# Optimization experiments

Hardware: AMD Instinct MI355X
Metric: run time of the kernel (lower is better)

## Reference

```python
import jax, jax.numpy as jnp
import numpy as np

VOCAB, D, E, I, L, B, T = 32000, 1024, 8, 2048, 2, 4, 2048
LN_EPS = 1e-5


def setup_inputs() -> dict:
    key = jax.random.key(0)
    ks = jax.random.split(key, 10)
    return {
        "x": jax.random.randint(ks[0], (B, T), 0, VOCAB),
        "emb": jax.random.normal(ks[1], (VOCAB, D), jnp.float32) * 0.02,
        "ln_g": jnp.ones((L, D), jnp.float32),
        "ln_b": jnp.zeros((L, D), jnp.float32),
        "gate_w": jax.random.normal(ks[2], (L, D, E), jnp.float32) * 0.02,
        "gate_b": jnp.zeros((L, E), jnp.float32),
        "w1": jax.random.normal(ks[3], (L, E, D, I), jnp.float32) * 0.02,
        "w2": jax.random.normal(ks[4], (L, E, I, D), jnp.float32) * 0.02,
        "head_w": jax.random.normal(ks[5], (D, VOCAB), jnp.float32) * 0.02,
        "head_b": jnp.zeros((VOCAB,), jnp.float32),
    }


def _layer_norm(h, g, b):
    mu = jnp.mean(h, axis=-1, keepdims=True)
    var = jnp.mean(jnp.square(h - mu), axis=-1, keepdims=True)
    return (h - mu) * jax.lax.rsqrt(var + LN_EPS) * g + b


def reference(x, emb, ln_g, ln_b, gate_w, gate_b, w1, w2, head_w, head_b):
    h = emb[x]  # [B,T,D]
    experts_all = []
    for l in range(ln_g.shape[0]):  # small fixed layer loop
        xn = _layer_norm(h, ln_g[l], ln_b[l])
        gating_logits = xn @ gate_w[l] + gate_b[l]          # [B,T,E]
        rw = jax.nn.softmax(gating_logits, axis=-1)
        e = jnp.einsum('btc,eci->btei', xn, w1[l])           # [B,T,E,I]
        e = jax.nn.gelu(e, approximate=False)                # torch F.gelu default = erf
        eo = jnp.einsum('btei,eic->btec', e, w2[l])          # [B,T,E,D]
        agg = jnp.einsum('btec,bte->btc', eo, rw)
        h = h + agg
        experts_all.append(eo)
    logits = h @ head_w + head_b                             # [B,T,VOCAB]
    return logits, jnp.stack(experts_all)                    # [L,B,T,E,D]
```

## Files before the change

kernel.cpp:

```cpp
#include <hip/hip_runtime.h>
#include <hip/hip_bf16.h>
#include <stdint.h>

#define NTOK 8192
#define DM   1024
#define NE   8
#define DI   2048
#define NL   2
#define NV   32000

typedef __attribute__((ext_vector_type(8))) __bf16 bf16x8;
typedef __attribute__((ext_vector_type(4))) float  f32x4;
typedef unsigned short u16;

__device__ __forceinline__ u16 f2bf(float f) {
  uint32_t u = __builtin_bit_cast(uint32_t, f);
  return (u16)((u + 0x7fffu + ((u >> 16) & 1u)) >> 16);
}

__device__ __forceinline__ void gload_lds16(const u16* g, void* l) {
  __builtin_amdgcn_global_load_lds(
      (const __attribute__((address_space(1))) void*)g,
      (__attribute__((address_space(3))) void*)l, 16, 0, 0);
}

__device__ __forceinline__ int xcd_swz(int orig, int nwg) {
  const int x = orig & 7, i = orig >> 3;
  const int q = nwg >> 3, r = nwg & 7;
  return (x < r ? x * (q + 1) : r * (q + 1) + (x - r) * q) + i;
}

template <int EPI>
__global__ __launch_bounds__(256, 2) void k_gemm(
    const u16* __restrict__ A0, const u16* __restrict__ W0,
    void* __restrict__ O0, const float* __restrict__ bias,
    int K, int mBlks, int nBlks,
    size_t aStride, size_t wStride, size_t oStride, int ldOut) {
  extern __shared__ char lds[];
  const int logical = xcd_swz(blockIdx.x, gridDim.x);
  const int perE = mBlks * nBlks;
  const int e    = logical / perE;
  const int rem  = logical - e * perE;
  const int nb   = rem / mBlks;
  const int mb   = rem - nb * mBlks;
  const int rowBase = mb * 128;
  const int colBase = nb * 256;
  const u16* A = A0 + (size_t)e * aStride;
  const u16* W = W0 + (size_t)e * wStride;

  const int t = threadIdx.x, lane = t & 63, wn = t >> 6;
  const int fr = lane & 15, kg = lane >> 4;

  const u16* gA[2]; int loA[2];
#pragma unroll
  for (int i = 0; i < 2; ++i) {
    const int c = t + 256 * i, row = c >> 2;
    const int gs = (c & 3) ^ ((row >> 2) & 3);
    gA[i] = A + (size_t)(rowBase + row) * K + gs * 8;
    loA[i] = c * 16;
  }
  const u16* gB[4]; int loB[4];
#pragma unroll
  for (int j = 0; j < 4; ++j) {
    const int c = t + 256 * j, row = c >> 2;
    const int gs = (c & 3) ^ ((row >> 2) & 3);
    gB[j] = W + (size_t)(colBase + row) * K + gs * 8;
    loB[j] = 8192 + c * 16;
  }

  auto stage = [&](int g, int buf) {
    char* dst = lds + buf * 24576;
#pragma unroll
    for (int i = 0; i < 2; ++i) gload_lds16(gA[i] + (size_t)g * 32, dst + loA[i]);
#pragma unroll
    for (int j = 0; j < 4; ++j) gload_lds16(gB[j] + (size_t)g * 32, dst + loB[j]);
  };

  const int swzo = (kg ^ ((fr >> 2) & 3)) * 16;
  const int aOff = fr * 64 + swzo;
  const int bOff = 8192 + (wn * 64 + fr) * 64 + swzo;

  f32x4 acc[8][4] = {};
  const int NG = K >> 5;

  auto compute = [&](int buf) {
    const char* base = lds + buf * 24576;
    bf16x8 af[8], bv[4];
#pragma unroll
    for (int mi = 0; mi < 8; ++mi) af[mi] = *(const bf16x8*)(base + aOff + mi * 1024);
#pragma unroll
    for (int ni = 0; ni < 4; ++ni) bv[ni] = *(const bf16x8*)(base + bOff + ni * 1024);
    __builtin_amdgcn_s_setprio(1);
#pragma unroll
    for (int mi = 0; mi < 8; ++mi)
#pragma unroll
      for (int ni = 0; ni < 4; ++ni)
        acc[mi][ni] = __builtin_amdgcn_mfma_f32_16x16x32_bf16(
            af[mi], bv[ni], acc[mi][ni], 0, 0, 0);
    __builtin_amdgcn_s_setprio(0);
  };

  stage(0, 0);
  stage(1, 1);

  int buf = 0;
#pragma unroll 1
  for (int g = 0; g < NG - 1; ++g) {
    asm volatile("s_waitcnt vmcnt(6)" ::: "memory");
    __builtin_amdgcn_s_barrier();
    asm volatile("" ::: "memory");
    if (g + 2 < NG) {
      int b2 = buf + 2; if (b2 >= 3) b2 -= 3;
      stage(g + 2, b2);
    }
    compute(buf);
    ++buf; if (buf >= 3) buf = 0;
  }
  asm volatile("s_waitcnt vmcnt(0)" ::: "memory");
  __builtin_amdgcn_s_barrier();
  asm volatile("" ::: "memory");
  compute(buf);

  const int row0 = rowBase + (kg << 2);
  const int col0 = colBase + wn * 64 + fr;
#pragma unroll
  for (int mi = 0; mi < 8; ++mi)
#pragma unroll
    for (int ni = 0; ni < 4; ++ni) {
      const int col = col0 + ni * 16;
      const int row = row0 + mi * 16;
      if (EPI == 0) {
        float* O = (float*)O0;
        const float bv2 = bias[col];
#pragma unroll
        for (int j = 0; j < 4; ++j)
          __builtin_nontemporal_store(acc[mi][ni][j] + bv2,
                                      &O[(size_t)(row + j) * ldOut + col]);
      } else if (EPI == 1) {
        u16* O = (u16*)O0 + (size_t)e * oStride;
#pragma unroll
        for (int j = 0; j < 4; ++j) {
          float v = acc[mi][ni][j];
          v = 0.5f * v * (1.0f + erff(v * 0.70710678118654752f));
          __builtin_nontemporal_store(f2bf(v), &O[(size_t)(row + j) * ldOut + col]);
        }
      } else {
        float* O = (float*)O0 + (size_t)e * oStride;
#pragma unroll
        for (int j = 0; j < 4; ++j)
          __builtin_nontemporal_store(acc[mi][ni][j],
                                      &O[(size_t)(row + j) * ldOut + col]);
      }
    }
}

__global__ void k_transcvt(const float* __restrict__ in, u16* __restrict__ out,
                           int R, int C) {
  const size_t bo = (size_t)blockIdx.z * R * C;
  in += bo; out += bo;
  __shared__ u16 tile[32][33];
  const int tx = threadIdx.x, ty = threadIdx.y;
  const int r0 = blockIdx.y << 5, c0 = blockIdx.x << 5;
#pragma unroll
  for (int j = 0; j < 4; ++j) {
    const int r = r0 + ty + j * 8;
    tile[ty + j * 8][tx] = f2bf(in[(size_t)r * C + c0 + tx]);
  }
  __syncthreads();
#pragma unroll
  for (int j = 0; j < 4; ++j) {
    const int c = c0 + ty + j * 8;
    out[(size_t)c * R + r0 + tx] = tile[tx][ty + j * 8];
  }
}

__global__ void k_gather(const int* __restrict__ x, const float* __restrict__ emb,
                         float* __restrict__ h) {
  const int n = blockIdx.x, t = threadIdx.x;
  const int id = x[n];
  ((float4*)(h + (size_t)n * DM))[t] = ((const float4*)(emb + (size_t)id * DM))[t];
}

__global__ void k_lngate(const float* __restrict__ h, const float* __restrict__ g,
                         const float* __restrict__ b, const float* __restrict__ gw,
                         const float* __restrict__ gb, u16* __restrict__ xnb,
                         float* __restrict__ rw) {
  const int n = blockIdx.x, t = threadIdx.x;
  const int wave = t >> 6, lane = t & 63;
  const float4 v = ((const float4*)(h + (size_t)n * DM))[t];
  float s = v.x + v.y + v.z + v.w;
  float q = v.x * v.x + v.y * v.y + v.z * v.z + v.w * v.w;
#pragma unroll
  for (int o = 32; o; o >>= 1) { s += __shfl_down(s, o, 64); q += __shfl_down(q, o, 64); }
  __shared__ float red[8];
  if (lane == 0) { red[wave] = s; red[wave + 4] = q; }
  __syncthreads();
  s = red[0] + red[1] + red[2] + red[3];
  q = red[4] + red[5] + red[6] + red[7];
  const float mu = s * (1.0f / DM);
  const float var = q * (1.0f / DM) - mu * mu;
  const float rs = rsqrtf(var + 1e-5f);
  const float4 gg = ((const float4*)g)[t];
  const float4 bb = ((const float4*)b)[t];
  float xv[4];
  xv[0] = (v.x - mu) * rs * gg.x + bb.x;
  xv[1] = (v.y - mu) * rs * gg.y + bb.y;
  xv[2] = (v.z - mu) * rs * gg.z + bb.z;
  xv[3] = (v.w - mu) * rs * gg.w + bb.w;
  ushort4 o4;
  o4.x = f2bf(xv[0]); o4.y = f2bf(xv[1]); o4.z = f2bf(xv[2]); o4.w = f2bf(xv[3]);
  ((ushort4*)(xnb + (size_t)n * DM))[t] = o4;
  float p[8];
#pragma unroll
  for (int e = 0; e < 8; ++e) p[e] = 0.0f;
  const float* gwp = gw + (size_t)t * 32;
#pragma unroll
  for (int j = 0; j < 4; ++j)
#pragma unroll
    for (int e = 0; e < 8; ++e) p[e] += xv[j] * gwp[j * 8 + e];
#pragma unroll
  for (int e = 0; e < 8; ++e)
#pragma unroll
    for (int o = 32; o; o >>= 1) p[e] += __shfl_down(p[e], o, 64);
  __shared__ float pr[4][8];
  if (lane == 0) {
#pragma unroll
    for (int e = 0; e < 8; ++e) pr[wave][e] = p[e];
  }
  __syncthreads();
  if (t == 0) {
    float lg[8], m = -1e30f;
#pragma unroll
    for (int e = 0; e < 8; ++e) {
      lg[e] = pr[0][e] + pr[1][e] + pr[2][e] + pr[3][e] + gb[e];
      m = fmaxf(m, lg[e]);
    }
    float ss = 0.0f;
#pragma unroll
    for (int e = 0; e < 8; ++e) { lg[e] = expf(lg[e] - m); ss += lg[e]; }
    const float inv = 1.0f / ss;
#pragma unroll
    for (int e = 0; e < 8; ++e) rw[(size_t)n * NE + e] = lg[e] * inv;
  }
}

__global__ void k_agg(float* __restrict__ h, u16* __restrict__ hbf,
                      const float* __restrict__ eo, const float* __restrict__ rw) {
  const int n = blockIdx.x, t = threadIdx.x;
  float w[8];
#pragma unroll
  for (int e = 0; e < 8; ++e) w[e] = rw[(size_t)n * NE + e];
  const f32x4* eo4 = (const f32x4*)(eo + (size_t)n * NE * DM);
  f32x4 a = ((f32x4*)(h + (size_t)n * DM))[t];
#pragma unroll
  for (int e = 0; e < 8; ++e) {
    const f32x4 xv = __builtin_nontemporal_load(&eo4[e * (DM / 4) + t]);
    a += w[e] * xv;
  }
  ((f32x4*)(h + (size_t)n * DM))[t] = a;
  ushort4 o4;
  o4.x = f2bf(a.x); o4.y = f2bf(a.y); o4.z = f2bf(a.z); o4.w = f2bf(a.w);
  ((ushort4*)(hbf + (size_t)n * DM))[t] = o4;
}

extern "C" void kernel_launch(void* const* d_in, const int* in_sizes, int n_in,
                              void* d_out, int out_size, void* d_ws, size_t ws_size,
                              hipStream_t stream) {
  const int*   x      = (const int*)d_in[0];
  const float* emb    = (const float*)d_in[1];
  const float* ln_g   = (const float*)d_in[2];
  const float* ln_b   = (const float*)d_in[3];
  const float* gate_w = (const float*)d_in[4];
  const float* gate_b = (const float*)d_in[5];
  const float* w1     = (const float*)d_in[6];
  const float* w2     = (const float*)d_in[7];
  const float* head_w = (const float*)d_in[8];
  const float* head_b = (const float*)d_in[9];

  float* logits  = (float*)d_out;
  float* experts = logits + (size_t)NTOK * NV;

  char* p = (char*)d_ws;
  auto carve = [&](size_t bytes) -> void* {
    void* r = (void*)p; p += (bytes + 255) & ~(size_t)255; return r;
  };
  float* h   = (float*)carve((size_t)NTOK * DM * 4);
  u16*   hbf = (u16*)  carve((size_t)NTOK * DM * 2);
  u16*   xnb = (u16*)  carve((size_t)NTOK * DM * 2);
  float* rw  = (float*)carve((size_t)NTOK * NE * 4);
  u16*   w1t = (u16*)  carve((size_t)NE * DM * DI * 2);
  u16*   w2t = (u16*)  carve((size_t)NE * DM * DI * 2);
  u16*   hwt = (u16*)  carve((size_t)NV * DM * 2);
  const size_t fixed = (size_t)(p - (char*)d_ws);
  const size_t eactOne = (size_t)NTOK * DI * 2;
  const bool batched = ws_size >= fixed + eactOne * NE;
  u16* eact = (u16*)carve(batched ? eactOne * NE : eactOne);

  const int LDSB = 73728;
  (void)hipFuncSetAttribute((const void*)k_gemm<0>,
                            hipFuncAttributeMaxDynamicSharedMemorySize, LDSB);
  (void)hipFuncSetAttribute((const void*)k_gemm<1>,
                            hipFuncAttributeMaxDynamicSharedMemorySize, LDSB);
  (void)hipFuncSetAttribute((const void*)k_gemm<2>,
                            hipFuncAttributeMaxDynamicSharedMemorySize, LDSB);

  const int MB = NTOK / 128;

  k_gather<<<dim3(NTOK), dim3(256), 0, stream>>>(x, emb, h);

  for (int l = 0; l < NL; ++l) {
    k_lngate<<<dim3(NTOK), dim3(256), 0, stream>>>(
        h, ln_g + (size_t)l * DM, ln_b + (size_t)l * DM,
        gate_w + (size_t)l * DM * NE, gate_b + (size_t)l * NE, xnb, rw);
    k_transcvt<<<dim3(DI / 32, DM / 32, NE), dim3(32, 8), 0, stream>>>(
        w1 + (size_t)l * NE * DM * DI, w1t, DM, DI);
    k_transcvt<<<dim3(DM / 32, DI / 32, NE), dim3(32, 8), 0, stream>>>(
        w2 + (size_t)l * NE * DM * DI, w2t, DI, DM);
    float* expertsL = experts + (size_t)l * NTOK * NE * DM;
    if (batched) {
      k_gemm<1><<<dim3(NE * MB * (DI / 256)), dim3(256), LDSB, stream>>>(
          xnb, w1t, eact, nullptr, DM, MB, DI / 256,
          (size_t)0, (size_t)DM * DI, (size_t)NTOK * DI, DI);
      k_gemm<2><<<dim3(NE * MB * (DM / 256)), dim3(256), LDSB, stream>>>(
          eact, w2t, expertsL, nullptr, DI, MB, DM / 256,
          (size_t)NTOK * DI, (size_t)DM * DI, (size_t)DM, NE * DM);
    } else {
      for (int e = 0; e < NE; ++e) {
        k_gemm<1><<<dim3(MB * (DI / 256)), dim3(256), LDSB, stream>>>(
            xnb, w1t + (size_t)e * DM * DI, eact, nullptr, DM, MB, DI / 256,
            (size_t)0, (size_t)0, (size_t)0, DI);
        k_gemm<2><<<dim3(MB * (DM / 256)), dim3(256), LDSB, stream>>>(
            eact, w2t + (size_t)e * DM * DI, expertsL + (size_t)e * DM, nullptr,
            DI, MB, DM / 256, (size_t)0, (size_t)0, (size_t)0, NE * DM);
      }
    }
    k_agg<<<dim3(NTOK), dim3(256), 0, stream>>>(h, hbf, expertsL, rw);
  }

  k_transcvt<<<dim3(NV / 32, DM / 32, 1), dim3(32, 8), 0, stream>>>(head_w, hwt, DM, NV);
  k_gemm<0><<<dim3(MB * (NV / 256)), dim3(256), LDSB, stream>>>(
      hbf, hwt, logits, head_b, DM, MB, NV / 256,
      (size_t)0, (size_t)0, (size_t)0, NV);
}
```

Measured before the change: 2.675 ms.

## Enlarge GEMM tile to 256x256 with 8 waves and 4-stage LDS pipeline

Replaces the 128x256 tile, 4-wave GEMM with a 256x256 tile computed by 8 waves (2x4 wave grid). Each block now reuses loaded A and B data across twice as many outputs, which halves global/L2 traffic per FLOP. The LDS pipeline grows from 3 to 4 buffers, the prefetch for the next stage is issued after the fragment reads, and block ordering changes to row-major over N. The cost is 128KB of LDS and one block per CU, which lowers occupancy and makes latency hiding depend on the deeper prefetch.

```diff
diff --git a/kernel.cpp b/kernel.cpp
--- a/kernel.cpp
+++ b/kernel.cpp
@@ -31,7 +31,7 @@
 }
 
 template <int EPI>
-__global__ __launch_bounds__(256, 2) void k_gemm(
+__global__ __launch_bounds__(512, 1) void k_gemm256(
     const u16* __restrict__ A0, const u16* __restrict__ W0,
     void* __restrict__ O0, const float* __restrict__ bias,
     int K, int mBlks, int nBlks,
@@ -41,55 +41,54 @@
   const int perE = mBlks * nBlks;
   const int e    = logical / perE;
   const int rem  = logical - e * perE;
-  const int nb   = rem / mBlks;
-  const int mb   = rem - nb * mBlks;
-  const int rowBase = mb * 128;
+  const int mb   = rem / nBlks;
+  const int nb   = rem - mb * nBlks;
+  const int rowBase = mb * 256;
   const int colBase = nb * 256;
   const u16* A = A0 + (size_t)e * aStride;
   const u16* W = W0 + (size_t)e * wStride;
 
-  const int t = threadIdx.x, lane = t & 63, wn = t >> 6;
+  const int t = threadIdx.x, lane = t & 63, wave = t >> 6;
+  const int wm = wave >> 2, wn = wave & 3;
   const int fr = lane & 15, kg = lane >> 4;
 
-  const u16* gA[2]; int loA[2];
+  const u16* gA[2]; const u16* gB[2]; int loA[2], loB[2];
 #pragma unroll
   for (int i = 0; i < 2; ++i) {
-    const int c = t + 256 * i, row = c >> 2;
+    const int c = t + 512 * i, row = c >> 2;
     const int gs = (c & 3) ^ ((row >> 2) & 3);
     gA[i] = A + (size_t)(rowBase + row) * K + gs * 8;
+    gB[i] = W + (size_t)(colBase + row) * K + gs * 8;
     loA[i] = c * 16;
-  }
-  const u16* gB[4]; int loB[4];
-#pragma unroll
-  for (int j = 0; j < 4; ++j) {
-    const int c = t + 256 * j, row = c >> 2;
-    const int gs = (c & 3) ^ ((row >> 2) & 3);
-    gB[j] = W + (size_t)(colBase + row) * K + gs * 8;
-    loB[j] = 8192 + c * 16;
-  }
-
-  auto stage = [&](int g, int buf) {
-    char* dst = lds + buf * 24576;
-#pragma unroll
-    for (int i = 0; i < 2; ++i) gload_lds16(gA[i] + (size_t)g * 32, dst + loA[i]);
-#pragma unroll
-    for (int j = 0; j < 4; ++j) gload_lds16(gB[j] + (size_t)g * 32, dst + loB[j]);
+    loB[i] = 16384 + c * 16;
+  }
+
+  auto stage = [&](int g) {
+    char* dst = lds + (g & 3) * 32768;
+#pragma unroll
+    for (int i = 0; i < 2; ++i) {
+      gload_lds16(gA[i] + (size_t)g * 32, dst + loA[i]);
+      gload_lds16(gB[i] + (size_t)g * 32, dst + loB[i]);
+    }
   };
 
   const int swzo = (kg ^ ((fr >> 2) & 3)) * 16;
-  const int aOff = fr * 64 + swzo;
-  const int bOff = 8192 + (wn * 64 + fr) * 64 + swzo;
+  const int aOff = (wm * 128 + fr) * 64 + swzo;
+  const int bOff = 16384 + (wn * 64 + fr) * 64 + swzo;
 
   f32x4 acc[8][4] = {};
   const int NG = K >> 5;
 
-  auto compute = [&](int buf) {
-    const char* base = lds + buf * 24576;
+  auto khalf = [&](int g, bool doStage) {
+    __builtin_amdgcn_s_barrier();
+    asm volatile("" ::: "memory");
+    const char* base = lds + (g & 3) * 32768;
     bf16x8 af[8], bv[4];
 #pragma unroll
     for (int mi = 0; mi < 8; ++mi) af[mi] = *(const bf16x8*)(base + aOff + mi * 1024);
 #pragma unroll
     for (int ni = 0; ni < 4; ++ni) bv[ni] = *(const bf16x8*)(base + bOff + ni * 1024);
+    if (doStage) stage(g + 3);
     __builtin_amdgcn_s_setprio(1);
 #pragma unroll
     for (int mi = 0; mi < 8; ++mi)
@@ -100,28 +99,21 @@
     __builtin_amdgcn_s_setprio(0);
   };
 
-  stage(0, 0);
-  stage(1, 1);
-
-  int buf = 0;
+  stage(0); stage(1); stage(2);
+
 #pragma unroll 1
-  for (int g = 0; g < NG - 1; ++g) {
-    asm volatile("s_waitcnt vmcnt(6)" ::: "memory");
-    __builtin_amdgcn_s_barrier();
-    asm volatile("" ::: "memory");
-    if (g + 2 < NG) {
-      int b2 = buf + 2; if (b2 >= 3) b2 -= 3;
-      stage(g + 2, b2);
-    }
-    compute(buf);
-    ++buf; if (buf >= 3) buf = 0;
-  }
+  for (int g = 0; g < NG - 3; ++g) {
+    asm volatile("s_waitcnt vmcnt(8)" ::: "memory");
+    khalf(g, true);
+  }
+  asm volatile("s_waitcnt vmcnt(8)" ::: "memory");
+  khalf(NG - 3, false);
+  asm volatile("s_waitcnt vmcnt(4)" ::: "memory");
+  khalf(NG - 2, false);
   asm volatile("s_waitcnt vmcnt(0)" ::: "memory");
-  __builtin_amdgcn_s_barrier();
-  asm volatile("" ::: "memory");
-  compute(buf);
-
-  const int row0 = rowBase + (kg << 2);
+  khalf(NG - 1, false);
+
+  const int row0 = rowBase + wm * 128 + (kg << 2);
   const int col0 = colBase + wn * 64 + fr;
 #pragma unroll
   for (int mi = 0; mi < 8; ++mi)
@@ -296,15 +288,15 @@
   const bool batched = ws_size >= fixed + eactOne * NE;
   u16* eact = (u16*)carve(batched ? eactOne * NE : eactOne);
 
-  const int LDSB = 73728;
-  (void)hipFuncSetAttribute((const void*)k_gemm<0>,
+  const int LDSB = 131072;
+  (void)hipFuncSetAttribute((const void*)k_gemm256<0>,
                             hipFuncAttributeMaxDynamicSharedMemorySize, LDSB);
-  (void)hipFuncSetAttribute((const void*)k_gemm<1>,
+  (void)hipFuncSetAttribute((const void*)k_gemm256<1>,
                             hipFuncAttributeMaxDynamicSharedMemorySize, LDSB);
-  (void)hipFuncSetAttribute((const void*)k_gemm<2>,
+  (void)hipFuncSetAttribute((const void*)k_gemm256<2>,
                             hipFuncAttributeMaxDynamicSharedMemorySize, LDSB);
 
-  const int MB = NTOK / 128;
+  const int MB = NTOK / 256;
 
   k_gather<<<dim3(NTOK), dim3(256), 0, stream>>>(x, emb, h);
 
@@ -318,18 +310,18 @@
         w2 + (size_t)l * NE * DM * DI, w2t, DI, DM);
     float* expertsL = experts + (size_t)l * NTOK * NE * DM;
     if (batched) {
-      k_gemm<1><<<dim3(NE * MB * (DI / 256)), dim3(256), LDSB, stream>>>(
+      k_gemm256<1><<<dim3(NE * MB * (DI / 256)), dim3(512), LDSB, stream>>>(
           xnb, w1t, eact, nullptr, DM, MB, DI / 256,
           (size_t)0, (size_t)DM * DI, (size_t)NTOK * DI, DI);
-      k_gemm<2><<<dim3(NE * MB * (DM / 256)), dim3(256), LDSB, stream>>>(
+      k_gemm256<2><<<dim3(NE * MB * (DM / 256)), dim3(512), LDSB, stream>>>(
           eact, w2t, expertsL, nullptr, DI, MB, DM / 256,
           (size_t)NTOK * DI, (size_t)DM * DI, (size_t)DM, NE * DM);
     } else {
       for (int e = 0; e < NE; ++e) {
-        k_gemm<1><<<dim3(MB * (DI / 256)), dim3(256), LDSB, stream>>>(
+        k_gemm256<1><<<dim3(MB * (DI / 256)), dim3(512), LDSB, stream>>>(
             xnb, w1t + (size_t)e * DM * DI, eact, nullptr, DM, MB, DI / 256,
             (size_t)0, (size_t)0, (size_t)0, DI);
-        k_gemm<2><<<dim3(MB * (DM / 256)), dim3(256), LDSB, stream>>>(
+        k_gemm256<2><<<dim3(MB * (DM / 256)), dim3(512), LDSB, stream>>>(
             eact, w2t + (size_t)e * DM * DI, expertsL + (size_t)e * DM, nullptr,
             DI, MB, DM / 256, (size_t)0, (size_t)0, (size_t)0, NE * DM);
       }
@@ -338,7 +330,7 @@
   }
 
   k_transcvt<<<dim3(NV / 32, DM / 32, 1), dim3(32, 8), 0, stream>>>(head_w, hwt, DM, NV);
-  k_gemm<0><<<dim3(MB * (NV / 256)), dim3(256), LDSB, stream>>>(
+  k_gemm256<0><<<dim3(MB * (NV / 256)), dim3(512), LDSB, stream>>>(
       hbf, hwt, logits, head_b, DM, MB, NV / 256,
       (size_t)0, (size_t)0, (size_t)0, NV);
 }
```

Result: faster. 2.514 ms (-6.0%).

## Stage GEMM epilogue through LDS for coalesced 128-bit nontemporal stores

Applied to the files above, without the earlier changes.

The GEMM epilogue now writes accumulators into LDS in two 64-row halves, then reads them back row-contiguously so each thread issues 16-byte nontemporal global stores. GELU, bf16 packing and bias add happen on the staged values. The old per-element scattered 4-byte and 2-byte stores wasted write bandwidth on the large fp32 expert outputs and logits. Block index decomposition is also switched so consecutive blocks walk along N instead of M. This adds LDS round trips and extra barriers, and the LDS reuse must fit the pipeline buffers.

```diff
diff --git a/kernel.cpp b/kernel.cpp
--- a/kernel.cpp
+++ b/kernel.cpp
@@ -11,11 +11,21 @@
 
 typedef __attribute__((ext_vector_type(8))) __bf16 bf16x8;
 typedef __attribute__((ext_vector_type(4))) float  f32x4;
+typedef __attribute__((ext_vector_type(4))) uint32_t u32x4;
 typedef unsigned short u16;
 
 __device__ __forceinline__ u16 f2bf(float f) {
   uint32_t u = __builtin_bit_cast(uint32_t, f);
   return (u16)((u + 0x7fffu + ((u >> 16) & 1u)) >> 16);
+}
+
+__device__ __forceinline__ void nts_f32x4(float* p, f32x4 v) {
+  asm volatile("global_store_dwordx4 %0, %1, off sc0 sc1 nt"
+               :: "v"(p), "v"(v) : "memory");
+}
+__device__ __forceinline__ void nts_b128(u16* p, u32x4 v) {
+  asm volatile("global_store_dwordx4 %0, %1, off sc0 sc1 nt"
+               :: "v"(p), "v"(v) : "memory");
 }
 
 __device__ __forceinline__ void gload_lds16(const u16* g, void* l) {
@@ -41,8 +51,8 @@
   const int perE = mBlks * nBlks;
   const int e    = logical / perE;
   const int rem  = logical - e * perE;
-  const int nb   = rem / mBlks;
-  const int mb   = rem - nb * mBlks;
+  const int mb   = rem / nBlks;
+  const int nb   = rem - mb * nBlks;
   const int rowBase = mb * 128;
   const int colBase = nb * 256;
   const u16* A = A0 + (size_t)e * aStride;
@@ -121,37 +131,62 @@
   asm volatile("" ::: "memory");
   compute(buf);
 
-  const int row0 = rowBase + (kg << 2);
-  const int col0 = colBase + wn * 64 + fr;
-#pragma unroll
-  for (int mi = 0; mi < 8; ++mi)
-#pragma unroll
-    for (int ni = 0; ni < 4; ++ni) {
-      const int col = col0 + ni * 16;
-      const int row = row0 + mi * 16;
-      if (EPI == 0) {
-        float* O = (float*)O0;
-        const float bv2 = bias[col];
+  float* ep = (float*)lds;
+  const int colL0 = wn * 64 + fr;
+  __syncthreads();
+#pragma unroll 1
+  for (int p = 0; p < 2; ++p) {
+#pragma unroll
+    for (int mm = 0; mm < 4; ++mm) {
+      const int mi = 4 * p + mm;
+#pragma unroll
+      for (int ni = 0; ni < 4; ++ni) {
+        const int rl = mm * 16 + (kg << 2);
+        const int cl = colL0 + ni * 16;
 #pragma unroll
         for (int j = 0; j < 4; ++j)
-          __builtin_nontemporal_store(acc[mi][ni][j] + bv2,
-                                      &O[(size_t)(row + j) * ldOut + col]);
-      } else if (EPI == 1) {
-        u16* O = (u16*)O0 + (size_t)e * oStride;
+          ep[(rl + j) * 256 + cl] = acc[mi][ni][j];
+      }
+    }
+    __syncthreads();
+    if (EPI == 1) {
+      u16* O = (u16*)O0 + (size_t)e * oStride;
+#pragma unroll
+      for (int ii = 0; ii < 8; ++ii) {
+        const int chunk = t + 256 * ii;
+        const int rl = chunk >> 5;
+        const int cl = (chunk & 31) << 3;
+        const f32x4 v0 = *(const f32x4*)(ep + rl * 256 + cl);
+        const f32x4 v1 = *(const f32x4*)(ep + rl * 256 + cl + 4);
+        float gv[8];
 #pragma unroll
         for (int j = 0; j < 4; ++j) {
-          float v = acc[mi][ni][j];
-          v = 0.5f * v * (1.0f + erff(v * 0.70710678118654752f));
-          __builtin_nontemporal_store(f2bf(v), &O[(size_t)(row + j) * ldOut + col]);
+          gv[j]     = 0.5f * v0[j] * (1.0f + erff(v0[j] * 0.70710678118654752f));
+          gv[4 + j] = 0.5f * v1[j] * (1.0f + erff(v1[j] * 0.70710678118654752f));
         }
-      } else {
-        float* O = (float*)O0 + (size_t)e * oStride;
-#pragma unroll
-        for (int j = 0; j < 4; ++j)
-          __builtin_nontemporal_store(acc[mi][ni][j],
-                                      &O[(size_t)(row + j) * ldOut + col]);
+        u32x4 pk;
+        pk.x = (uint32_t)f2bf(gv[0]) | ((uint32_t)f2bf(gv[1]) << 16);
+        pk.y = (uint32_t)f2bf(gv[2]) | ((uint32_t)f2bf(gv[3]) << 16);
+        pk.z = (uint32_t)f2bf(gv[4]) | ((uint32_t)f2bf(gv[5]) << 16);
+        pk.w = (uint32_t)f2bf(gv[6]) | ((uint32_t)f2bf(gv[7]) << 16);
+        const int row = rowBase + p * 64 + rl;
+        nts_b128(&O[(size_t)row * ldOut + colBase + cl], pk);
       }
-    }
+    } else {
+      float* O = (float*)O0 + (EPI == 2 ? (size_t)e * oStride : (size_t)0);
+#pragma unroll
+      for (int ii = 0; ii < 16; ++ii) {
+        const int chunk = t + 256 * ii;
+        const int rl = chunk >> 6;
+        const int cl = (chunk & 63) << 2;
+        f32x4 v = *(const f32x4*)(ep + rl * 256 + cl);
+        if (EPI == 0) v += *(const f32x4*)(bias + colBase + cl);
+        const int row = rowBase + p * 64 + rl;
+        nts_f32x4(&O[(size_t)row * ldOut + colBase + cl], v);
+      }
+    }
+    __syncthreads();
+  }
 }
 
 __global__ void k_transcvt(const float* __restrict__ in, u16* __restrict__ out,
```

New measurement: 3.983 ms. 1.49x slower.
